# Performance work log

Hardware: AMD Instinct MI355X
Metric: run time of the kernel (lower is better)

Reference implementation:

```python
import jax, jax.numpy as jnp
import numpy as np
from jax import lax

B, NE, ZD, GAMMA, BETA = 16384, 512, 32, 0.99, 1.0

def conv2d(x, w, b, stride, pad):
    y = lax.conv_general_dilated(x, w, (stride, stride), [(pad, pad), (pad, pad)],
                                 dimension_numbers=('NCHW', 'OIHW', 'NCHW'))
    return y if b is None else y + b[None, :, None, None]

def convt2d(x, w, b, stride, pad):
    # torch ConvTranspose2d(w: [in,out,kh,kw]) == dilated conv with flipped, transposed kernel
    k = w.shape[2]
    wf = jnp.flip(w, (2, 3)).transpose(1, 0, 2, 3)  # -> [out,in,kh,kw]
    p = k - 1 - pad
    y = lax.conv_general_dilated(x, wf, (1, 1), [(p, p), (p, p)], lhs_dilation=(stride, stride),
                                 dimension_numbers=('NCHW', 'OIHW', 'NCHW'))
    return y + b[None, :, None, None]

def res_stack(x, w1, w2):
    # ResidualLayer: relu -> conv3x3 (32->64) -> relu -> conv1x1 (64->32), add; stack ends with relu
    r = jax.nn.relu(x)
    r = conv2d(r, w1, None, 1, 1)
    r = jax.nn.relu(r)
    r = conv2d(r, w2, None, 1, 0)
    return jax.nn.relu(x + r)

def linear(x, w, b):
    return x @ w.T + b

def setup_inputs() -> dict:
    key = jax.random.key(0)
    ks = jax.random.split(key, 24)
    g = lambda k, s, sc=0.05: (jax.random.normal(k, s) * sc).astype(jnp.float32)
    inp = {
        'x': jax.random.uniform(ks[0], (B, 1, 28, 28), dtype=jnp.float32),
        'conv1_w': g(ks[1], (16, 1, 4, 4)), 'conv1_b': jnp.zeros((16,), jnp.float32),
        'conv2_w': g(ks[2], (32, 16, 4, 4)), 'conv2_b': jnp.zeros((32,), jnp.float32),
        'res1_w1': g(ks[3], (64, 32, 3, 3)), 'res1_w2': g(ks[4], (32, 64, 1, 1)),
        'fc1_w': g(ks[5], (224, 1568)), 'fc1_b': jnp.zeros((224,), jnp.float32),
        'fc2_w': g(ks[6], (ZD, 224)), 'fc2_b': jnp.zeros((ZD,), jnp.float32),
        'emb': jax.random.uniform(ks[7], (NE, ZD), jnp.float32, -1.0 / NE, 1.0 / NE),
        'n_mat': jnp.ones((NE,), jnp.float32),
        'm_mat': jnp.ones((NE, ZD), jnp.float32),
        'fc3_w': g(ks[8], (224, ZD)), 'fc3_b': jnp.zeros((224,), jnp.float32),
        'fc4_w': g(ks[9], (1568, 224)), 'fc4_b': jnp.zeros((1568,), jnp.float32),
        'res2_w1': g(ks[10], (64, 32, 3, 3)), 'res2_w2': g(ks[11], (32, 64, 1, 1)),
        'convt1_w': g(ks[12], (32, 16, 4, 4)), 'convt1_b': jnp.zeros((16,), jnp.float32),
        'convt2_w': g(ks[13], (16, 1, 4, 4)), 'convt2_b': jnp.zeros((1,), jnp.float32),
    }
    return inp

def vq(z, emb, n_mat, m_mat):
    # z: [N, ZD]; nearest-codeword assignment
    d = (jnp.sum(z * z, 1, keepdims=True) + jnp.sum(emb * emb, 1)
         - 2.0 * (z @ emb.T))                                   # [N, NE]
    idx = jnp.argmin(d, axis=1)                                  # [N]
    z_q = jnp.take(emb, idx, axis=0)                             # [N, ZD]
    counts = jax.ops.segment_sum(jnp.ones((z.shape[0],), z.dtype), idx, num_segments=NE)
    sums = jax.ops.segment_sum(lax.stop_gradient(z), idx, num_segments=NE)
    n_new = n_mat * GAMMA + counts * (1.0 - GAMMA)
    m_new = m_mat * GAMMA + sums * (1.0 - GAMMA)
    emb_new = m_new / n_new[:, None]
    commit_loss = BETA * jnp.mean((lax.stop_gradient(z_q) - z) ** 2)
    quant_loss = jnp.mean((z_q - lax.stop_gradient(z)) ** 2)
    z_q_st = z + lax.stop_gradient(z_q - z)                      # straight-through
    e_mean = counts / z.shape[0]
    perplexity = jnp.exp(-jnp.sum(e_mean * jnp.log(e_mean + 1e-10)))
    return quant_loss, commit_loss, z_q_st, perplexity, emb_new

def reference(x, conv1_w, conv1_b, conv2_w, conv2_b, res1_w1, res1_w2,
              fc1_w, fc1_b, fc2_w, fc2_b, emb, n_mat, m_mat,
              fc3_w, fc3_b, fc4_w, fc4_b, res2_w1, res2_w2,
              convt1_w, convt1_b, convt2_w, convt2_b):
    # encoder: 28x28 -> 14x14 -> 7x7
    h = jax.nn.relu(conv2d(x, conv1_w, conv1_b, 2, 1))
    h = conv2d(h, conv2_w, conv2_b, 2, 1)
    h = res_stack(h, res1_w1, res1_w2)
    h = h.reshape(h.shape[0], -1)                                # [B, 1568]
    h = jax.nn.relu(linear(h, fc1_w, fc1_b))
    z = linear(h, fc2_w, fc2_b)                                  # [B, ZD]
    quant_loss, commit_loss, z_q, perplexity, emb_new = vq(z, emb, n_mat, m_mat)
    # decoder
    h = jax.nn.relu(linear(z_q, fc3_w, fc3_b))
    h = jax.nn.relu(linear(h, fc4_w, fc4_b))
    h = h.reshape(-1, 32, 7, 7)
    h = res_stack(h, res2_w1, res2_w2)
    h = jax.nn.relu(convt2d(h, convt1_w, convt1_b, 2, 1))
    x_rec = convt2d(h, convt2_w, convt2_b, 2, 1)                 # [B,1,28,28]
    return x_rec, quant_loss, commit_loss, perplexity, emb_new
```

## Files before the change

### kernel.cpp

```cpp
#include <hip/hip_runtime.h>
#include <math.h>

#define NB 16384
typedef unsigned short ushort_t;
typedef unsigned int uint_t;
typedef __attribute__((ext_vector_type(8))) short short8;
typedef __attribute__((ext_vector_type(4))) float fx4;
typedef _Float16 half2v __attribute__((ext_vector_type(2)));
typedef _Float16 half4v __attribute__((ext_vector_type(4)));

static const size_t OFF_HB    = 0;
static const size_t OFF_F1B   = 12845056;
static const size_t OFF_F3B   = 14680064;
static const size_t OFF_Z     = 16515072;
static const size_t OFF_IDX   = 17039360;
static const size_t OFF_ZQB   = 17055744;
static const size_t OFF_CNT   = 17317888;
static const size_t OFF_SUM   = 17318400;
static const size_t OFF_LOSS  = 17334784;
static const size_t OFF_WENC  = 17334848;
static const size_t OFF_WT1B  = 17343040;
static const size_t OFF_WR1B  = 17351232;
static const size_t OFF_WR2B  = 17360448;
static const size_t OFF_W2B1  = 17369664;
static const size_t OFF_W2B2  = 17370688;
static const size_t OFF_FC1WB = 17371712;
static const size_t OFF_FC2WB = 17547328;
static const size_t OFF_FC3WB = 17550912;
static const size_t OFF_FC4WB = 17554496;
static const size_t OFF_FC4BP = 17730112;

static __device__ __forceinline__ ushort_t f2bf(float f) {
  union { float f; uint_t u; } v; v.f = f;
  return (ushort_t)((v.u + 0x7fffu + ((v.u >> 16) & 1u)) >> 16);
}
static __device__ __forceinline__ float bf2f(ushort_t h) {
  union { uint_t u; float f; } v; v.u = ((uint_t)h) << 16;
  return v.f;
}
static __device__ __forceinline__ float fdot2(half2v a, half2v b, float c) {
#if __has_builtin(__builtin_amdgcn_fdot2)
  return __builtin_amdgcn_fdot2(a, b, c, false);
#else
  return c + (float)a.x * (float)b.x + (float)a.y * (float)b.y;
#endif
}

__global__ __launch_bounds__(256) void k_prep(
    const float* __restrict__ c2w, const float* __restrict__ r1w1,
    const float* __restrict__ r1w2, const float* __restrict__ r2w1,
    const float* __restrict__ r2w2, const float* __restrict__ t1w,
    const float* __restrict__ fc1w, const float* __restrict__ fc2w,
    const float* __restrict__ fc3w, const float* __restrict__ fc4w,
    const float* __restrict__ fc4b, float* __restrict__ ws)
{
  int gid = blockIdx.x * 256 + threadIdx.x;
  if (gid == 0) ws[OFF_LOSS] = 0.f;
  if (gid >= 775712) return;
  ushort_t* wencb = (ushort_t*)(ws + OFF_WENC);
  ushort_t* wt1b  = (ushort_t*)(ws + OFF_WT1B);
  ushort_t* wr1b  = (ushort_t*)(ws + OFF_WR1B);
  ushort_t* wr2b  = (ushort_t*)(ws + OFF_WR2B);
  ushort_t* w2b1  = (ushort_t*)(ws + OFF_W2B1);
  ushort_t* w2b2  = (ushort_t*)(ws + OFF_W2B2);
  ushort_t* fc1wb = (ushort_t*)(ws + OFF_FC1WB);
  ushort_t* fc2wb = (ushort_t*)(ws + OFF_FC2WB);
  ushort_t* fc3wb = (ushort_t*)(ws + OFF_FC3WB);
  ushort_t* fc4wb = (ushort_t*)(ws + OFF_FC4WB);
  float*    fc4bp = ws + OFF_FC4BP;
  int i = gid;
  if (i < 8192) {
    int kidx = i & 31, rest = i >> 5, co = rest & 31, kb = rest >> 5;
    int ky = kb >> 1, k2 = kb & 1, kxs = kidx >> 4, ci = kidx & 15;
    wencb[i] = f2bf(c2w[co*256 + ci*16 + ky*4 + 2*k2 + kxs]);
  } else if (i < 16384) {
    int j = i - 8192, ci = j & 31, rest = j >> 5, co = rest & 15, kk = rest >> 4;
    wt1b[j] = f2bf(t1w[ci*256 + co*16 + kk]);
  } else if (i < 34816) {
    int j = i - 16384, ci = j & 31, r = j >> 5, co = r & 63, kk = r >> 6;
    wr1b[j] = f2bf(r1w1[co*288 + ci*9 + kk]);
  } else if (i < 53248) {
    int j = i - 34816, ci = j & 31, r = j >> 5, co = r & 63, kk = r >> 6;
    wr2b[j] = f2bf(r2w1[co*288 + ci*9 + kk]);
  } else if (i < 55296) {
    int j = i - 53248; w2b1[j] = f2bf(r1w2[j]);
  } else if (i < 57344) {
    int j = i - 55296; w2b2[j] = f2bf(r2w2[j]);
  } else if (i < 408576) {
    int j = i - 57344, n = j / 1568, k = j % 1568;
    int p = k >> 5, ci = k & 31;
    fc1wb[j] = f2bf(fc1w[n*1568 + ci*49 + p]);
  } else if (i < 415744) {
    int j = i - 408576; fc2wb[j] = f2bf(fc2w[j]);
  } else if (i < 422912) {
    int j = i - 415744; fc3wb[j] = f2bf(fc3w[j]);
  } else if (i < 774144) {
    int j = i - 422912, np = j / 224, k = j % 224;
    int p = np >> 5, ci = np & 31;
    fc4wb[j] = f2bf(fc4w[(ci*49 + p)*224 + k]);
  } else {
    int np = i - 774144, p = np >> 5, ci = np & 31;
    fc4bp[np] = fc4b[ci*49 + p];
  }
}

__global__ __launch_bounds__(256) void k_enc(const float* __restrict__ x,
    const float* __restrict__ w1, const float* __restrict__ b1,
    const ushort_t* __restrict__ wencb, const float* __restrict__ b2,
    ushort_t* __restrict__ hb)
{
  __shared__ float xin[30][32];
  __shared__ ushort_t ph1b[256*24];
  __shared__ ushort_t outl[1568];
  int b = blockIdx.x, t = threadIdx.x, l = t & 63, w = t >> 6;
  int pr = l & 15, g = l >> 4;
  int co16 = t & 15;
  float wr1v[16];
  #pragma unroll
  for (int kk = 0; kk < 16; ++kk) wr1v[kk] = w1[co16*16 + kk];
  float bv1 = b1[co16];
  short8 bf[8][2];
  #pragma unroll
  for (int kb = 0; kb < 8; ++kb)
    #pragma unroll
    for (int nt = 0; nt < 2; ++nt)
      bf[kb][nt] = *(const short8*)(wencb + (size_t)(kb*32 + nt*16 + pr)*32 + g*8);
  uint_t* pz = (uint_t*)ph1b;
  for (int i = t; i < 3072; i += 256) pz[i] = 0;
  float* xp = &xin[0][0];
  for (int i = t; i < 960; i += 256) xp[i] = 0.f;
  __syncthreads();
  const float* xb = x + (size_t)b*784;
  for (int i = t; i < 784; i += 256) xin[i/28 + 1][i%28 + 1] = xb[i];
  __syncthreads();
  char* phc = (char*)ph1b;
  for (int i = t; i < 3136; i += 256) {
    int p = i >> 4, oy = p/14, ox = p%14;
    float acc = bv1;
    #pragma unroll
    for (int ky = 0; ky < 4; ++ky)
      #pragma unroll
      for (int kx = 0; kx < 4; ++kx)
        acc += xin[2*oy+ky][2*ox+kx] * wr1v[ky*4+kx];
    *(ushort_t*)(phc + ((oy+1)*16 + (ox+1))*48 + co16*2) = f2bf(fmaxf(acc, 0.f));
  }
  __syncthreads();
  int p = w*16 + pr; if (p > 48) p = 48;
  int oy = p/7, ox = p%7;
  fx4 acc2[2];
  acc2[0] = (fx4){0.f,0.f,0.f,0.f}; acc2[1] = (fx4){0.f,0.f,0.f,0.f};
  #pragma unroll
  for (int kb = 0; kb < 8; ++kb) {
    int ky = kb >> 1, k2 = kb & 1;
    int prow = (2*oy + ky)*16 + 2*ox + 2*k2 + (g >> 1);
    short8 afr = *(const short8*)(phc + prow*48 + (g & 1)*16);
    acc2[0] = __builtin_amdgcn_mfma_f32_16x16x32_bf16(afr, bf[kb][0], acc2[0], 0, 0, 0);
    acc2[1] = __builtin_amdgcn_mfma_f32_16x16x32_bf16(afr, bf[kb][1], acc2[1], 0, 0, 0);
  }
  #pragma unroll
  for (int nt = 0; nt < 2; ++nt) {
    int co = nt*16 + pr;
    float bv = b2[co];
    #pragma unroll
    for (int i = 0; i < 4; ++i) {
      int pix = w*16 + g*4 + i;
      if (pix < 49) outl[pix*32 + co] = f2bf(acc2[nt][i] + bv);
    }
  }
  __syncthreads();
  uint_t* dst = (uint_t*)(hb + (size_t)b*1568);
  const uint_t* so = (const uint_t*)outl;
  for (int j = t; j < 784; j += 256) dst[j] = so[j];
}

__global__ __launch_bounds__(256) void k_res(ushort_t* __restrict__ hb,
    const ushort_t* __restrict__ wrb, const ushort_t* __restrict__ w2b)
{
  __shared__ ushort_t pinT[3456];
  __shared__ ushort_t rl[4096];
  __shared__ ushort_t hrawb[1568];
  __shared__ ushort_t outl[1568];
  int b = blockIdx.x, t = threadIdx.x, l = t & 63, w = t >> 6, g = l >> 4;

  short8 bfr[9];
  #pragma unroll
  for (int o = 0; o < 9; ++o)
    bfr[o] = *(const short8*)(wrb + (size_t)(o*64 + w*16 + (l & 15))*32 + g*8);

  uint_t* pz = (uint_t*)pinT;
  for (int i = t; i < 1728; i += 256) pz[i] = 0;
  __syncthreads();

  const uint_t* src = (const uint_t*)(hb + (size_t)b*1568);
  char* pinc = (char*)pinT;
  for (int j = t; j < 784; j += 256) {
    uint_t u = src[j];
    ((uint_t*)hrawb)[j] = u;
    uint_t ur = u;
    ur = (ur & 0x80000000u) ? (ur & 0x0000ffffu) : ur;
    ur = (ur & 0x8000u)     ? (ur & 0xffff0000u) : ur;
    int p = j >> 4, c2 = (j & 15) << 1;
    int ppix = (p/7 + 1)*12 + (p%7) + 1;
    int byte = ((ppix << 6) + (c2 << 1)) ^ ((ppix & 6) << 3);
    *(uint_t*)(pinc + byte) = ur;
  }
  __syncthreads();

  fx4 acc[4];
  #pragma unroll
  for (int mt = 0; mt < 4; ++mt) acc[mt] = (fx4){0.f, 0.f, 0.f, 0.f};
  int pb[4];
  #pragma unroll
  for (int mt = 0; mt < 4; ++mt) {
    int p = mt*16 + (l & 15); if (p > 48) p = 48;
    pb[mt] = (p / 7)*12 + (p % 7);
  }
  #pragma unroll
  for (int mt = 0; mt < 4; ++mt) {
    #pragma unroll
    for (int o = 0; o < 9; ++o) {
      int ppix = pb[mt] + (o / 3)*12 + (o % 3);
      int byte = ((ppix << 6) + (g << 4)) ^ ((ppix & 6) << 3);
      short8 afr = *(const short8*)(pinc + byte);
      acc[mt] = __builtin_amdgcn_mfma_f32_16x16x32_bf16(afr, bfr[o], acc[mt], 0, 0, 0);
    }
  }
  char* rlc = (char*)rl;
  #pragma unroll
  for (int mt = 0; mt < 4; ++mt) {
    #pragma unroll
    for (int i = 0; i < 4; ++i) {
      int pixr = mt*16 + g*4 + i;
      int co2 = w*16 + (l & 15);
      int byte = ((pixr << 7) + (co2 << 1)) ^ ((pixr & 7) << 4);
      *(ushort_t*)(rlc + byte) = f2bf(fmaxf(acc[mt][i], 0.f));
    }
  }
  __syncthreads();

  fx4 a1[2];
  a1[0] = (fx4){0.f,0.f,0.f,0.f}; a1[1] = (fx4){0.f,0.f,0.f,0.f};
  int prr = w*16 + (l & 15);
  #pragma unroll
  for (int kf = 0; kf < 2; ++kf) {
    int byte = ((prr << 7) + (kf << 6) + (g << 4)) ^ ((prr & 7) << 4);
    short8 ar = *(const short8*)(rlc + byte);
    #pragma unroll
    for (int nt = 0; nt < 2; ++nt) {
      short8 br = *(const short8*)(w2b + (size_t)(nt*16 + (l & 15))*64 + kf*32 + g*8);
      a1[nt] = __builtin_amdgcn_mfma_f32_16x16x32_bf16(ar, br, a1[nt], 0, 0, 0);
    }
  }
  #pragma unroll
  for (int nt = 0; nt < 2; ++nt) {
    #pragma unroll
    for (int i = 0; i < 4; ++i) {
      int pix = w*16 + g*4 + i;
      if (pix < 49) {
        int co2 = nt*16 + (l & 15);
        int idx2 = pix*32 + co2;
        float v = bf2f(hrawb[idx2]) + a1[nt][i];
        outl[idx2] = f2bf(fmaxf(v, 0.f));
      }
    }
  }
  __syncthreads();
  uint_t* dst = (uint_t*)(hb + (size_t)b*1568);
  const uint_t* so = (const uint_t*)outl;
  for (int j = t; j < 784; j += 256) dst[j] = so[j];
}

template<int BNF, bool OUTBF16, bool RELU>
__global__ __launch_bounds__(256) void k_mm(const ushort_t* __restrict__ A,
    const ushort_t* __restrict__ Wb, const float* __restrict__ bias,
    void* __restrict__ C, int M, int N, int K)
{
  __shared__ ushort_t As[2048];
  int t = threadIdx.x, l = t & 63, w = t >> 6, g = l >> 4;
  int m0 = blockIdx.x * 64, n0 = blockIdx.y * (BNF * 16);
  fx4 acc[BNF];
  #pragma unroll
  for (int nt = 0; nt < BNF; ++nt) acc[nt] = (fx4){0.f, 0.f, 0.f, 0.f};
  char* asc = (char*)As;
  int srow = t >> 2, sks = (t & 3) * 8;
  int sbyte = ((srow << 6) + (sks << 1)) ^ ((srow & 6) << 3);
  int arow = w*16 + (l & 15);
  int abyte = ((arow << 6) + (g << 4)) ^ ((arow & 6) << 3);
  const ushort_t* ap = A + (size_t)(m0 + srow)*K + sks;
  short8 av = *(const short8*)ap;
  for (int k0 = 0; k0 < K; k0 += 32) {
    __syncthreads();
    *(short8*)(asc + sbyte) = av;
    __syncthreads();
    if (k0 + 32 < K) av = *(const short8*)(ap + k0 + 32);
    short8 afr = *(const short8*)(asc + abyte);
    #pragma unroll
    for (int nt = 0; nt < BNF; ++nt) {
      short8 bfr = *(const short8*)(Wb + (size_t)(n0 + nt*16 + (l & 15))*K + k0 + g*8);
      acc[nt] = __builtin_amdgcn_mfma_f32_16x16x32_bf16(afr, bfr, acc[nt], 0, 0, 0);
    }
  }
  #pragma unroll
  for (int nt = 0; nt < BNF; ++nt) {
    int col = n0 + nt*16 + (l & 15);
    float bv = bias[col];
    #pragma unroll
    for (int i = 0; i < 4; ++i) {
      int row = m0 + w*16 + g*4 + i;
      float v = acc[nt][i] + bv;
      if (RELU) v = fmaxf(v, 0.f);
      if (OUTBF16) ((ushort_t*)C)[(size_t)row*N + col] = f2bf(v);
      else         ((float*)C)[(size_t)row*N + col] = v;
    }
  }
}

__global__ __launch_bounds__(256) void k_vq_assign(const float* __restrict__ z,
    const float* __restrict__ emb, ushort_t* __restrict__ zqb, int* __restrict__ idx,
    float* __restrict__ loss)
{
  __shared__ float esq[512];
  int t = threadIdx.x;
  int n = blockIdx.x * 256 + t;
  for (int e = t; e < 512; e += 256) {
    const float4* ep = (const float4*)&emb[e*32];
    float s = 0.f;
    #pragma unroll
    for (int q = 0; q < 8; ++q) { float4 v = ep[q]; s += v.x*v.x + v.y*v.y + v.z*v.z + v.w*v.w; }
    esq[e] = s;
  }
  __syncthreads();
  float zv[32];
  const float4* zp = (const float4*)&z[n*32];
  float zz = 0.f;
  #pragma unroll
  for (int q = 0; q < 8; ++q) {
    float4 v = zp[q];
    zv[4*q]=v.x; zv[4*q+1]=v.y; zv[4*q+2]=v.z; zv[4*q+3]=v.w;
    zz += v.x*v.x + v.y*v.y + v.z*v.z + v.w*v.w;
  }
  float best = 3.4e38f; int bi = 0;
  for (int e = 0; e < 512; ++e) {
    const float4* ep = (const float4*)&emb[e*32];
    float dot = 0.f;
    #pragma unroll
    for (int q = 0; q < 8; ++q) {
      float4 v = ep[q];
      dot += zv[4*q]*v.x + zv[4*q+1]*v.y + zv[4*q+2]*v.z + zv[4*q+3]*v.w;
    }
    float d = zz + esq[e] - 2.f*dot;
    if (d < best) { best = d; bi = e; }
  }
  idx[n] = bi;
  const float4* bp = (const float4*)&emb[bi*32];
  uint_t* zo = (uint_t*)(zqb + (size_t)n*32);
  float ls = 0.f;
  #pragma unroll
  for (int q = 0; q < 8; ++q) {
    float4 v = bp[q];
    zo[q*2]   = (uint_t)f2bf(v.x) | ((uint_t)f2bf(v.y) << 16);
    zo[q*2+1] = (uint_t)f2bf(v.z) | ((uint_t)f2bf(v.w) << 16);
    float d0 = v.x - zv[4*q], d1 = v.y - zv[4*q+1];
    float d2 = v.z - zv[4*q+2], d3 = v.w - zv[4*q+3];
    ls += d0*d0 + d1*d1 + d2*d2 + d3*d3;
  }
  #pragma unroll
  for (int m = 32; m >= 1; m >>= 1) ls += __shfl_xor(ls, m);
  if ((t & 63) == 0) atomicAdd(loss, ls);
}

__global__ __launch_bounds__(64) void k_vq_reduce(const int* __restrict__ idx,
    const float* __restrict__ z, float* __restrict__ counts, float* __restrict__ sums)
{
  int e = blockIdx.x, t = threadIdx.x;
  float cnt = 0.f, sv[32];
  #pragma unroll
  for (int k = 0; k < 32; ++k) sv[k] = 0.f;
  for (int n = t; n < 16384; n += 64) {
    if (idx[n] == e) {
      cnt += 1.f;
      const float4* zp = (const float4*)&z[n*32];
      #pragma unroll
      for (int q = 0; q < 8; ++q) {
        float4 v = zp[q];
        sv[4*q] += v.x; sv[4*q+1] += v.y; sv[4*q+2] += v.z; sv[4*q+3] += v.w;
      }
    }
  }
  #pragma unroll
  for (int m = 32; m >= 1; m >>= 1) {
    cnt += __shfl_xor(cnt, m);
    #pragma unroll
    for (int k = 0; k < 32; ++k) sv[k] += __shfl_xor(sv[k], m);
  }
  if (t == 0) {
    counts[e] = cnt;
    #pragma unroll
    for (int k = 0; k < 32; ++k) sums[e*32 + k] = sv[k];
  }
}

__global__ __launch_bounds__(512) void k_vq_final(const float* __restrict__ counts,
    const float* __restrict__ sums, const float* __restrict__ n_mat,
    const float* __restrict__ m_mat, const float* __restrict__ loss,
    float* __restrict__ out)
{
  __shared__ float red[8];
  int t = threadIdx.x;
  float c = counts[t];
  float nn = n_mat[t]*0.99f + c*0.01f;
  #pragma unroll
  for (int k = 0; k < 32; ++k) {
    float mn = m_mat[t*32+k]*0.99f + sums[t*32+k]*0.01f;
    out[12845059 + t*32 + k] = mn / nn;
  }
  float em = c * (1.f/16384.f);
  float ht = em * logf(em + 1e-10f);
  #pragma unroll
  for (int m = 32; m >= 1; m >>= 1) ht += __shfl_xor(ht, m);
  if ((t & 63) == 0) red[t >> 6] = ht;
  __syncthreads();
  if (t == 0) {
    float H = 0.f;
    #pragma unroll
    for (int i = 0; i < 8; ++i) H += red[i];
    float q = loss[0] * (1.f/524288.f);
    out[12845056] = q;
    out[12845057] = q;
    out[12845058] = expf(-H);
  }
}

__global__ __launch_bounds__(256) void k_dec(const ushort_t* __restrict__ h5,
    const ushort_t* __restrict__ wt1b, const float* __restrict__ bt1,
    const float* __restrict__ wt2, const float* __restrict__ bt2,
    float* __restrict__ out)
{
  __shared__ ushort_t pinT[3456];
  __shared__ ushort_t pt1b[256*20];
  __shared__ float w2l[256];
  __shared__ float outl[784];
  int b = blockIdx.x, t = threadIdx.x, l = t & 63, w = t >> 6;
  int pr = l & 15, g = l >> 4;
  int py = w >> 1, px = w & 1;
  short8 bfr[4];
  #pragma unroll
  for (int r = 0; r < 2; ++r)
    #pragma unroll
    for (int c = 0; c < 2; ++c) {
      int kk = (3 - py - 2*r)*4 + (3 - px - 2*c);
      bfr[r*2 + c] = *(const short8*)(wt1b + (size_t)(kk*16 + pr)*32 + g*8);
    }
  uint_t* pz = (uint_t*)pinT;
  for (int i = t; i < 1728; i += 256) pz[i] = 0;
  uint_t* qz = (uint_t*)pt1b;
  for (int i = t; i < 2560; i += 256) qz[i] = 0;
  if (t < 256) w2l[t] = wt2[t];
  __syncthreads();
  const uint_t* src = (const uint_t*)(h5 + (size_t)b*1568);
  char* pinc = (char*)pinT;
  for (int j = t; j < 784; j += 256) {
    uint_t u = src[j];
    int p = j >> 4, c2 = (j & 15) << 1;
    int ppix = (p/7 + 1)*12 + (p%7) + 1;
    int byte = ((ppix << 6) + (c2 << 1)) ^ ((ppix & 6) << 3);
    *(uint_t*)(pinc + byte) = u;
  }
  __syncthreads();
  fx4 acc[4];
  #pragma unroll
  for (int mt = 0; mt < 4; ++mt) acc[mt] = (fx4){0.f, 0.f, 0.f, 0.f};
  int pb[4];
  #pragma unroll
  for (int mt = 0; mt < 4; ++mt) {
    int p = mt*16 + pr; if (p > 48) p = 48;
    pb[mt] = (p / 7)*12 + (p % 7);
  }
  #pragma unroll
  for (int mt = 0; mt < 4; ++mt) {
    #pragma unroll
    for (int r = 0; r < 2; ++r)
      #pragma unroll
      for (int c = 0; c < 2; ++c) {
        int ppix = pb[mt] + (py + r)*12 + (px + c);
        int byte = ((ppix << 6) + (g << 4)) ^ ((ppix & 6) << 3);
        short8 afr = *(const short8*)(pinc + byte);
        acc[mt] = __builtin_amdgcn_mfma_f32_16x16x32_bf16(afr, bfr[r*2 + c], acc[mt], 0, 0, 0);
      }
  }
  char* ptc = (char*)pt1b;
  float bv1 = bt1[pr];
  #pragma unroll
  for (int mt = 0; mt < 4; ++mt) {
    #pragma unroll
    for (int i = 0; i < 4; ++i) {
      int p = mt*16 + g*4 + i;
      if (p < 49) {
        int yy = p / 7, xx = p % 7;
        int opix = (2*yy + py + 1)*16 + (2*xx + px + 1);
        *(_Float16*)(ptc + opix*40 + pr*2) = (_Float16)(fmaxf(acc[mt][i] + bv1, 0.f));
      }
    }
  }
  __syncthreads();
  {
    int qy = w >> 1, qx = w & 1;
    int kkt[4] = { qy*4 + qx, qy*4 + qx + 2, (qy+2)*4 + qx, (qy+2)*4 + qx + 2 };
    half2v wh[4][8];
    #pragma unroll
    for (int tt = 0; tt < 4; ++tt)
      #pragma unroll
      for (int q = 0; q < 8; ++q) {
        wh[tt][q].x = (_Float16)w2l[(2*q)*16 + kkt[tt]];
        wh[tt][q].y = (_Float16)w2l[(2*q+1)*16 + kkt[tt]];
      }
    float bv2 = bt2[0];
    #pragma unroll
    for (int k = 0; k < 4; ++k) {
      int j = l + k*64;
      if (j < 196) {
        int a = j / 14, bb = j % 14;
        int oy = 2*a + 1 - qy, ox = 2*bb + 1 - qx;
        int iy1 = a + 1 - qy, iy2 = a - qy;
        int ix1 = bb + 1 - qx, ix2 = bb - qx;
        int prw[4];
        prw[0] = (iy1 + 1)*16 + (ix1 + 1);
        prw[1] = (iy1 + 1)*16 + (ix2 + 1);
        prw[2] = (iy2 + 1)*16 + (ix1 + 1);
        prw[3] = (iy2 + 1)*16 + (ix2 + 1);
        float s = bv2;
        #pragma unroll
        for (int tt = 0; tt < 4; ++tt) {
          const char* base = ptc + prw[tt]*40;
          #pragma unroll
          for (int jj = 0; jj < 2; ++jj) {
            half4v a4 = *(const half4v*)(base + jj*8);
            half4v b4 = *(const half4v*)(base + 16 + jj*8);
            half2v a0 = {a4.x, a4.y}, a1 = {a4.z, a4.w};
            half2v b0 = {b4.x, b4.y}, b1 = {b4.z, b4.w};
            s = fdot2(a0, wh[tt][jj*2],     s);
            s = fdot2(a1, wh[tt][jj*2 + 1], s);
            s = fdot2(b0, wh[tt][jj*2 + 4], s);
            s = fdot2(b1, wh[tt][jj*2 + 5], s);
          }
        }
        outl[oy*28 + ox] = s;
      }
    }
  }
  __syncthreads();
  float* dst = out + (size_t)b*784;
  for (int i = t; i < 784; i += 256) dst[i] = outl[i];
}

extern "C" void kernel_launch(void* const* d_in, const int* in_sizes, int n_in,
                              void* d_out, int out_size, void* d_ws, size_t ws_size,
                              hipStream_t stream)
{
  const float* x    = (const float*)d_in[0];
  const float* c1w  = (const float*)d_in[1];
  const float* c1b  = (const float*)d_in[2];
  const float* c2w  = (const float*)d_in[3];
  const float* c2b  = (const float*)d_in[4];
  const float* r1w1 = (const float*)d_in[5];
  const float* r1w2 = (const float*)d_in[6];
  const float* fc1w = (const float*)d_in[7];
  const float* fc1b = (const float*)d_in[8];
  const float* fc2w = (const float*)d_in[9];
  const float* fc2b = (const float*)d_in[10];
  const float* emb  = (const float*)d_in[11];
  const float* nmat = (const float*)d_in[12];
  const float* mmat = (const float*)d_in[13];
  const float* fc3w = (const float*)d_in[14];
  const float* fc3b = (const float*)d_in[15];
  const float* fc4w = (const float*)d_in[16];
  const float* fc4b = (const float*)d_in[17];
  const float* r2w1 = (const float*)d_in[18];
  const float* r2w2 = (const float*)d_in[19];
  const float* t1w  = (const float*)d_in[20];
  const float* t1b  = (const float*)d_in[21];
  const float* t2w  = (const float*)d_in[22];
  const float* t2b  = (const float*)d_in[23];
  float* ws  = (float*)d_ws;
  float* out = (float*)d_out;

  ushort_t* hb   = (ushort_t*)(ws + OFF_HB);
  ushort_t* f1b  = (ushort_t*)(ws + OFF_F1B);
  ushort_t* f3b  = (ushort_t*)(ws + OFF_F3B);
  float*    z    = ws + OFF_Z;
  int*      idx  = (int*)(ws + OFF_IDX);
  ushort_t* zqb  = (ushort_t*)(ws + OFF_ZQB);
  float*    cnts = ws + OFF_CNT;
  float*    sums = ws + OFF_SUM;
  float*    loss = ws + OFF_LOSS;
  ushort_t* wencb = (ushort_t*)(ws + OFF_WENC);
  ushort_t* wt1b  = (ushort_t*)(ws + OFF_WT1B);
  ushort_t* wr1b  = (ushort_t*)(ws + OFF_WR1B);
  ushort_t* wr2b  = (ushort_t*)(ws + OFF_WR2B);
  ushort_t* w2b1  = (ushort_t*)(ws + OFF_W2B1);
  ushort_t* w2b2  = (ushort_t*)(ws + OFF_W2B2);
  ushort_t* fc1wb = (ushort_t*)(ws + OFF_FC1WB);
  ushort_t* fc2wb = (ushort_t*)(ws + OFF_FC2WB);
  ushort_t* fc3wb = (ushort_t*)(ws + OFF_FC3WB);
  ushort_t* fc4wb = (ushort_t*)(ws + OFF_FC4WB);
  float*    fc4bp = ws + OFF_FC4BP;

  k_prep<<<3031, 256, 0, stream>>>(c2w, r1w1, r1w2, r2w1, r2w2, t1w,
                                   fc1w, fc2w, fc3w, fc4w, fc4b, ws);
  k_enc<<<NB, 256, 0, stream>>>(x, c1w, c1b, wencb, c2b, hb);
  k_res<<<NB, 256, 0, stream>>>(hb, wr1b, w2b1);
  k_mm<14, true, true><<<dim3(256, 1), 256, 0, stream>>>(hb, fc1wb, fc1b, f1b, 16384, 224, 1568);
  k_mm<2, false, false><<<dim3(256, 1), 256, 0, stream>>>(f1b, fc2wb, fc2b, z, 16384, 32, 224);
  k_vq_assign<<<64, 256, 0, stream>>>(z, emb, zqb, idx, loss);
  k_vq_reduce<<<512, 64, 0, stream>>>(idx, z, cnts, sums);
  k_vq_final<<<1, 512, 0, stream>>>(cnts, sums, nmat, mmat, loss, out);
  k_mm<14, true, true><<<dim3(256, 1), 256, 0, stream>>>(zqb, fc3wb, fc3b, f3b, 16384, 224, 32);
  k_mm<14, true, true><<<dim3(256, 7), 256, 0, stream>>>(f3b, fc4wb, fc4bp, hb, 16384, 1568, 224);
  k_res<<<NB, 256, 0, stream>>>(hb, wr2b, w2b2);
  k_dec<<<NB, 256, 0, stream>>>(hb, wt1b, t1b, t2w, t2b, out);
}
```

Before: 994.3 us.

## Use MFMA for encoder conv1 and parallelize VQ assignment across wavefront lanes

The first encoder convolution now builds a bf16 im2col tile in swizzled shared memory and runs it as a 16x16x32 MFMA against a prepacked, zero-padded conv1 weight matrix, replacing the scalar FMA loop. The VQ nearest-codebook search changes from one thread per sample over 64 blocks to one wavefront per sample over 4096 blocks. Each lane scores 8 codes and the wave does a shuffle argmin with lowest-index tie-break. The goal is to remove the heavily underoccupied serial VQ kernel and the scalar conv work, at the cost of recomputing codebook norms per wave and running conv1 in bf16.

```diff
diff --git a/kernel.cpp b/kernel.cpp
--- a/kernel.cpp
+++ b/kernel.cpp
@@ -29,6 +29,7 @@
 static const size_t OFF_FC3WB = 17550912;
 static const size_t OFF_FC4WB = 17554496;
 static const size_t OFF_FC4BP = 17730112;
+static const size_t OFF_WENC1 = 17731680;
 
 static __device__ __forceinline__ ushort_t f2bf(float f) {
   union { float f; uint_t u; } v; v.f = f;
@@ -47,16 +48,17 @@
 }
 
 __global__ __launch_bounds__(256) void k_prep(
-    const float* __restrict__ c2w, const float* __restrict__ r1w1,
-    const float* __restrict__ r1w2, const float* __restrict__ r2w1,
-    const float* __restrict__ r2w2, const float* __restrict__ t1w,
+    const float* __restrict__ c1w, const float* __restrict__ c2w,
+    const float* __restrict__ r1w1, const float* __restrict__ r1w2,
+    const float* __restrict__ r2w1, const float* __restrict__ r2w2,
+    const float* __restrict__ t1w,
     const float* __restrict__ fc1w, const float* __restrict__ fc2w,
     const float* __restrict__ fc3w, const float* __restrict__ fc4w,
     const float* __restrict__ fc4b, float* __restrict__ ws)
 {
   int gid = blockIdx.x * 256 + threadIdx.x;
   if (gid == 0) ws[OFF_LOSS] = 0.f;
-  if (gid >= 775712) return;
+  if (gid >= 776224) return;
   ushort_t* wencb = (ushort_t*)(ws + OFF_WENC);
   ushort_t* wt1b  = (ushort_t*)(ws + OFF_WT1B);
   ushort_t* wr1b  = (ushort_t*)(ws + OFF_WR1B);
@@ -68,6 +70,7 @@
   ushort_t* fc3wb = (ushort_t*)(ws + OFF_FC3WB);
   ushort_t* fc4wb = (ushort_t*)(ws + OFF_FC4WB);
   float*    fc4bp = ws + OFF_FC4BP;
+  ushort_t* wenc1b = (ushort_t*)(ws + OFF_WENC1);
   int i = gid;
   if (i < 8192) {
     int kidx = i & 31, rest = i >> 5, co = rest & 31, kb = rest >> 5;
@@ -98,33 +101,36 @@
     int j = i - 422912, np = j / 224, k = j % 224;
     int p = np >> 5, ci = np & 31;
     fc4wb[j] = f2bf(fc4w[(ci*49 + p)*224 + k]);
-  } else {
+  } else if (i < 775712) {
     int np = i - 774144, p = np >> 5, ci = np & 31;
     fc4bp[np] = fc4b[ci*49 + p];
+  } else {
+    int j = i - 775712, k = j & 31, co = j >> 5;
+    wenc1b[j] = (k < 16) ? f2bf(c1w[co*16 + k]) : (ushort_t)0;
   }
 }
 
 __global__ __launch_bounds__(256) void k_enc(const float* __restrict__ x,
-    const float* __restrict__ w1, const float* __restrict__ b1,
+    const ushort_t* __restrict__ wenc1b, const float* __restrict__ b1,
     const ushort_t* __restrict__ wencb, const float* __restrict__ b2,
     ushort_t* __restrict__ hb)
 {
   __shared__ float xin[30][32];
+  __shared__ ushort_t icb[208*32];
   __shared__ ushort_t ph1b[256*24];
   __shared__ ushort_t outl[1568];
   int b = blockIdx.x, t = threadIdx.x, l = t & 63, w = t >> 6;
   int pr = l & 15, g = l >> 4;
-  int co16 = t & 15;
-  float wr1v[16];
-  #pragma unroll
-  for (int kk = 0; kk < 16; ++kk) wr1v[kk] = w1[co16*16 + kk];
-  float bv1 = b1[co16];
+  short8 bf1 = *(const short8*)(wenc1b + (size_t)pr*32 + g*8);
   short8 bf[8][2];
   #pragma unroll
   for (int kb = 0; kb < 8; ++kb)
     #pragma unroll
     for (int nt = 0; nt < 2; ++nt)
       bf[kb][nt] = *(const short8*)(wencb + (size_t)(kb*32 + nt*16 + pr)*32 + g*8);
+  float bv1 = b1[pr];
+  uint_t* iz = (uint_t*)icb;
+  for (int i = t; i < 3328; i += 256) iz[i] = 0;
   uint_t* pz = (uint_t*)ph1b;
   for (int i = t; i < 3072; i += 256) pz[i] = 0;
   float* xp = &xin[0][0];
@@ -133,16 +139,33 @@
   const float* xb = x + (size_t)b*784;
   for (int i = t; i < 784; i += 256) xin[i/28 + 1][i%28 + 1] = xb[i];
   __syncthreads();
+  char* icc = (char*)icb;
+  for (int i = t; i < 3136; i += 256) {
+    int p = i >> 4, k = i & 15;
+    int oy = p / 14, ox = p % 14;
+    float v = xin[2*oy + (k >> 2)][2*ox + (k & 3)];
+    int byte = ((p << 6) + (k << 1)) ^ ((p & 6) << 3);
+    *(ushort_t*)(icc + byte) = f2bf(v);
+  }
+  __syncthreads();
   char* phc = (char*)ph1b;
-  for (int i = t; i < 3136; i += 256) {
-    int p = i >> 4, oy = p/14, ox = p%14;
-    float acc = bv1;
-    #pragma unroll
-    for (int ky = 0; ky < 4; ++ky)
-      #pragma unroll
-      for (int kx = 0; kx < 4; ++kx)
-        acc += xin[2*oy+ky][2*ox+kx] * wr1v[ky*4+kx];
-    *(ushort_t*)(phc + ((oy+1)*16 + (ox+1))*48 + co16*2) = f2bf(fmaxf(acc, 0.f));
+  #pragma unroll
+  for (int mq = 0; mq < 4; ++mq) {
+    int mt = w + mq*4;
+    if (mt > 12) continue;
+    fx4 a1 = (fx4){0.f, 0.f, 0.f, 0.f};
+    int arow = mt*16 + pr;
+    int byte = ((arow << 6) + (g << 4)) ^ ((arow & 6) << 3);
+    short8 af = *(const short8*)(icc + byte);
+    a1 = __builtin_amdgcn_mfma_f32_16x16x32_bf16(af, bf1, a1, 0, 0, 0);
+    #pragma unroll
+    for (int i = 0; i < 4; ++i) {
+      int pix = mt*16 + g*4 + i;
+      if (pix < 196) {
+        int prow = (pix/14 + 1)*16 + (pix%14) + 1;
+        *(ushort_t*)(phc + prow*48 + pr*2) = f2bf(fmaxf(a1[i] + bv1, 0.f));
+      }
+    }
   }
   __syncthreads();
   int p = w*16 + pr; if (p > 48) p = 48;
@@ -319,19 +342,11 @@
     const float* __restrict__ emb, ushort_t* __restrict__ zqb, int* __restrict__ idx,
     float* __restrict__ loss)
 {
-  __shared__ float esq[512];
-  int t = threadIdx.x;
-  int n = blockIdx.x * 256 + t;
-  for (int e = t; e < 512; e += 256) {
-    const float4* ep = (const float4*)&emb[e*32];
-    float s = 0.f;
-    #pragma unroll
-    for (int q = 0; q < 8; ++q) { float4 v = ep[q]; s += v.x*v.x + v.y*v.y + v.z*v.z + v.w*v.w; }
-    esq[e] = s;
-  }
-  __syncthreads();
+  __shared__ float lred[4];
+  int t = threadIdx.x, w = t >> 6, ln = t & 63;
+  int n = blockIdx.x * 4 + w;
   float zv[32];
-  const float4* zp = (const float4*)&z[n*32];
+  const float4* zp = (const float4*)&z[(size_t)n*32];
   float zz = 0.f;
   #pragma unroll
   for (int q = 0; q < 8; ++q) {
@@ -339,34 +354,40 @@
     zv[4*q]=v.x; zv[4*q+1]=v.y; zv[4*q+2]=v.z; zv[4*q+3]=v.w;
     zz += v.x*v.x + v.y*v.y + v.z*v.z + v.w*v.w;
   }
-  float best = 3.4e38f; int bi = 0;
-  for (int e = 0; e < 512; ++e) {
-    const float4* ep = (const float4*)&emb[e*32];
-    float dot = 0.f;
+  float best = 3.4e38f; int bi = 0x7fffffff;
+  #pragma unroll
+  for (int c = 0; c < 8; ++c) {
+    int e = c*64 + ln;
+    const float4* ep = (const float4*)&emb[(size_t)e*32];
+    float dot = 0.f, es = 0.f;
     #pragma unroll
     for (int q = 0; q < 8; ++q) {
       float4 v = ep[q];
       dot += zv[4*q]*v.x + zv[4*q+1]*v.y + zv[4*q+2]*v.z + zv[4*q+3]*v.w;
-    }
-    float d = zz + esq[e] - 2.f*dot;
+      es  += v.x*v.x + v.y*v.y + v.z*v.z + v.w*v.w;
+    }
+    float d = zz + es - 2.f*dot;
     if (d < best) { best = d; bi = e; }
   }
-  idx[n] = bi;
-  const float4* bp = (const float4*)&emb[bi*32];
-  uint_t* zo = (uint_t*)(zqb + (size_t)n*32);
+  #pragma unroll
+  for (int m = 32; m >= 1; m >>= 1) {
+    float ob = __shfl_xor(best, m);
+    int   oi = __shfl_xor(bi, m);
+    if (ob < best || (ob == best && oi < bi)) { best = ob; bi = oi; }
+  }
+  if (ln == 0) idx[n] = bi;
+  int dim = ln & 31;
+  float ev = emb[(size_t)bi*32 + dim];
+  float evh = __shfl_xor(ev, 1);
+  if (ln < 32 && !(ln & 1))
+    ((uint_t*)(zqb + (size_t)n*32))[ln >> 1] = (uint_t)f2bf(ev) | ((uint_t)f2bf(evh) << 16);
   float ls = 0.f;
-  #pragma unroll
-  for (int q = 0; q < 8; ++q) {
-    float4 v = bp[q];
-    zo[q*2]   = (uint_t)f2bf(v.x) | ((uint_t)f2bf(v.y) << 16);
-    zo[q*2+1] = (uint_t)f2bf(v.z) | ((uint_t)f2bf(v.w) << 16);
-    float d0 = v.x - zv[4*q], d1 = v.y - zv[4*q+1];
-    float d2 = v.z - zv[4*q+2], d3 = v.w - zv[4*q+3];
-    ls += d0*d0 + d1*d1 + d2*d2 + d3*d3;
-  }
+  if (ln < 32) { float d = ev - z[(size_t)n*32 + dim]; ls = d*d; }
   #pragma unroll
   for (int m = 32; m >= 1; m >>= 1) ls += __shfl_xor(ls, m);
-  if ((t & 63) == 0) atomicAdd(loss, ls);
+  if (ln == 0) lred[w] = ls;
+  __syncthreads();
+  if (t == 0) atomicAdd(loss, lred[0] + lred[1] + lred[2] + lred[3]);
 }
 
 __global__ __launch_bounds__(64) void k_vq_reduce(const int* __restrict__ idx,
@@ -593,25 +614,26 @@
   float*    cnts = ws + OFF_CNT;
   float*    sums = ws + OFF_SUM;
   float*    loss = ws + OFF_LOSS;
-  ushort_t* wencb = (ushort_t*)(ws + OFF_WENC);
-  ushort_t* wt1b  = (ushort_t*)(ws + OFF_WT1B);
-  ushort_t* wr1b  = (ushort_t*)(ws + OFF_WR1B);
-  ushort_t* wr2b  = (ushort_t*)(ws + OFF_WR2B);
-  ushort_t* w2b1  = (ushort_t*)(ws + OFF_W2B1);
-  ushort_t* w2b2  = (ushort_t*)(ws + OFF_W2B2);
-  ushort_t* fc1wb = (ushort_t*)(ws + OFF_FC1WB);
-  ushort_t* fc2wb = (ushort_t*)(ws + OFF_FC2WB);
-  ushort_t* fc3wb = (ushort_t*)(ws + OFF_FC3WB);
-  ushort_t* fc4wb = (ushort_t*)(ws + OFF_FC4WB);
-  float*    fc4bp = ws + OFF_FC4BP;
-
-  k_prep<<<3031, 256, 0, stream>>>(c2w, r1w1, r1w2, r2w1, r2w2, t1w,
+  ushort_t* wencb  = (ushort_t*)(ws + OFF_WENC);
+  ushort_t* wenc1b = (ushort_t*)(ws + OFF_WENC1);
+  ushort_t* wt1b   = (ushort_t*)(ws + OFF_WT1B);
+  ushort_t* wr1b   = (ushort_t*)(ws + OFF_WR1B);
+  ushort_t* wr2b   = (ushort_t*)(ws + OFF_WR2B);
+  ushort_t* w2b1   = (ushort_t*)(ws + OFF_W2B1);
+  ushort_t* w2b2   = (ushort_t*)(ws + OFF_W2B2);
+  ushort_t* fc1wb  = (ushort_t*)(ws + OFF_FC1WB);
+  ushort_t* fc2wb  = (ushort_t*)(ws + OFF_FC2WB);
+  ushort_t* fc3wb  = (ushort_t*)(ws + OFF_FC3WB);
+  ushort_t* fc4wb  = (ushort_t*)(ws + OFF_FC4WB);
+  float*    fc4bp  = ws + OFF_FC4BP;
+
+  k_prep<<<3033, 256, 0, stream>>>(c1w, c2w, r1w1, r1w2, r2w1, r2w2, t1w,
                                    fc1w, fc2w, fc3w, fc4w, fc4b, ws);
-  k_enc<<<NB, 256, 0, stream>>>(x, c1w, c1b, wencb, c2b, hb);
+  k_enc<<<NB, 256, 0, stream>>>(x, wenc1b, c1b, wencb, c2b, hb);
   k_res<<<NB, 256, 0, stream>>>(hb, wr1b, w2b1);
   k_mm<14, true, true><<<dim3(256, 1), 256, 0, stream>>>(hb, fc1wb, fc1b, f1b, 16384, 224, 1568);
   k_mm<2, false, false><<<dim3(256, 1), 256, 0, stream>>>(f1b, fc2wb, fc2b, z, 16384, 32, 224);
-  k_vq_assign<<<64, 256, 0, stream>>>(z, emb, zqb, idx, loss);
+  k_vq_assign<<<4096, 256, 0, stream>>>(z, emb, zqb, idx, loss);
   k_vq_reduce<<<512, 64, 0, stream>>>(idx, z, cnts, sums);
   k_vq_final<<<1, 512, 0, stream>>>(cnts, sums, nmat, mmat, loss, out);
   k_mm<14, true, true><<<dim3(256, 1), 256, 0, stream>>>(zqb, fc3wb, fc3b, f3b, 16384, 224, 32);
```

Measured after the change: 1.029 ms. 1.03x slower.

## Split VQ codebook search across warps with LDS-staged embeddings

Applied to the files above, without the earlier changes.

The nearest-codebook search now launches 256 blocks of 512 threads instead of 64 blocks of 256. The full embedding table and a 64-row tile of z are staged in shared memory. Each of 8 wavefronts scans 64 codes for the same 64 rows, and the partial argmins are merged in LDS with ties broken toward the lower index. This targets the previous low occupancy, where each thread serially scanned 512 codes from global memory. In exchange it uses about 70KB of LDS per block and adds several barriers.

```diff
diff --git a/kernel.cpp b/kernel.cpp
--- a/kernel.cpp
+++ b/kernel.cpp
@@ -315,58 +315,87 @@
   }
 }
 
-__global__ __launch_bounds__(256) void k_vq_assign(const float* __restrict__ z,
+__global__ __launch_bounds__(512) void k_vq_assign(const float* __restrict__ z,
     const float* __restrict__ emb, ushort_t* __restrict__ zqb, int* __restrict__ idx,
     float* __restrict__ loss)
 {
+  __shared__ float embL[16384];
   __shared__ float esq[512];
-  int t = threadIdx.x;
-  int n = blockIdx.x * 256 + t;
-  for (int e = t; e < 512; e += 256) {
-    const float4* ep = (const float4*)&emb[e*32];
+  __shared__ float zL[64*33];
+  __shared__ float bestdL[8][64];
+  __shared__ int   bestiL[8][64];
+  int t = threadIdx.x, r = t & 63, q = t >> 6;
+  int n0 = blockIdx.x * 64;
+  fx4* embL4 = (fx4*)embL;
+  const fx4* emb4 = (const fx4*)emb;
+  #pragma unroll
+  for (int j = 0; j < 8; ++j) embL4[t + j*512] = emb4[t + j*512];
+  {
+    int f0 = t*4;
+    int row = f0 >> 5, col = f0 & 31;
+    const float4 v = *(const float4*)&z[(size_t)n0*32 + f0];
+    zL[row*33 + col]   = v.x; zL[row*33 + col+1] = v.y;
+    zL[row*33 + col+2] = v.z; zL[row*33 + col+3] = v.w;
+  }
+  __syncthreads();
+  {
     float s = 0.f;
-    #pragma unroll
-    for (int q = 0; q < 8; ++q) { float4 v = ep[q]; s += v.x*v.x + v.y*v.y + v.z*v.z + v.w*v.w; }
-    esq[e] = s;
-  }
-  __syncthreads();
+    const fx4* ep = (const fx4*)&embL[t*32 & 16383];
+    #pragma unroll
+    for (int j2 = 0; j2 < 8; ++j2) { fx4 v = ep[j2]; s += v.x*v.x + v.y*v.y + v.z*v.z + v.w*v.w; }
+    esq[t & 511] = s;
+  }
   float zv[32];
-  const float4* zp = (const float4*)&z[n*32];
-  float zz = 0.f;
-  #pragma unroll
-  for (int q = 0; q < 8; ++q) {
-    float4 v = zp[q];
-    zv[4*q]=v.x; zv[4*q+1]=v.y; zv[4*q+2]=v.z; zv[4*q+3]=v.w;
-    zz += v.x*v.x + v.y*v.y + v.z*v.z + v.w*v.w;
-  }
+  #pragma unroll
+  for (int k = 0; k < 32; ++k) zv[k] = zL[r*33 + k];
+  __syncthreads();
   float best = 3.4e38f; int bi = 0;
-  for (int e = 0; e < 512; ++e) {
-    const float4* ep = (const float4*)&emb[e*32];
+  for (int j = 0; j < 64; ++j) {
+    int e = q*64 + j;
+    const fx4* ep = (const fx4*)&embL[e*32];
     float dot = 0.f;
     #pragma unroll
-    for (int q = 0; q < 8; ++q) {
-      float4 v = ep[q];
-      dot += zv[4*q]*v.x + zv[4*q+1]*v.y + zv[4*q+2]*v.z + zv[4*q+3]*v.w;
-    }
-    float d = zz + esq[e] - 2.f*dot;
+    for (int k2 = 0; k2 < 8; ++k2) {
+      fx4 v = ep[k2];
+      dot += zv[4*k2]*v.x + zv[4*k2+1]*v.y + zv[4*k2+2]*v.z + zv[4*k2+3]*v.w;
+    }
+    float d = esq[e] - 2.f*dot;
     if (d < best) { best = d; bi = e; }
   }
-  idx[n] = bi;
-  const float4* bp = (const float4*)&emb[bi*32];
-  uint_t* zo = (uint_t*)(zqb + (size_t)n*32);
-  float ls = 0.f;
-  #pragma unroll
-  for (int q = 0; q < 8; ++q) {
-    float4 v = bp[q];
-    zo[q*2]   = (uint_t)f2bf(v.x) | ((uint_t)f2bf(v.y) << 16);
-    zo[q*2+1] = (uint_t)f2bf(v.z) | ((uint_t)f2bf(v.w) << 16);
-    float d0 = v.x - zv[4*q], d1 = v.y - zv[4*q+1];
-    float d2 = v.z - zv[4*q+2], d3 = v.w - zv[4*q+3];
-    ls += d0*d0 + d1*d1 + d2*d2 + d3*d3;
-  }
-  #pragma unroll
-  for (int m = 32; m >= 1; m >>= 1) ls += __shfl_xor(ls, m);
-  if ((t & 63) == 0) atomicAdd(loss, ls);
+  bestdL[q][r] = best; bestiL[q][r] = bi;
+  __syncthreads();
+  if (t < 64) {
+    float bb = bestdL[0][r]; int bbi = bestiL[0][r];
+    #pragma unroll
+    for (int j = 1; j < 8; ++j) {
+      float d = bestdL[j][r]; int di = bestiL[j][r];
+      if (d < bb || (d == bb && di < bbi)) { bb = d; bbi = di; }
+    }
+    idx[n0 + r] = bbi;
+    bestiL[0][r] = bbi;
+  }
+  __syncthreads();
+  if (t < 256) {
+    int q4 = t >> 6;
+    int n = n0 + r;
+    int bsel = bestiL[0][r];
+    float ls = 0.f;
+    uint_t ow[4];
+    #pragma unroll
+    for (int h = 0; h < 4; ++h) {
+      float e0 = embL[bsel*32 + q4*8 + 2*h];
+      float e1 = embL[bsel*32 + q4*8 + 2*h + 1];
+      float d0 = e0 - zv[q4*8 + 2*h], d1 = e1 - zv[q4*8 + 2*h + 1];
+      ls += d0*d0 + d1*d1;
+      ow[h] = (uint_t)f2bf(e0) | ((uint_t)f2bf(e1) << 16);
+    }
+    uint_t* zo = (uint_t*)(zqb + (size_t)n*32) + q4*4;
+    #pragma unroll
+    for (int h = 0; h < 4; ++h) zo[h] = ow[h];
+    #pragma unroll
+    for (int m = 32; m >= 1; m >>= 1) ls += __shfl_xor(ls, m);
+    if (r == 0) atomicAdd(loss, ls);
+  }
 }
 
 __global__ __launch_bounds__(64) void k_vq_reduce(const int* __restrict__ idx,
@@ -593,17 +622,17 @@
   float*    cnts = ws + OFF_CNT;
   float*    sums = ws + OFF_SUM;
   float*    loss = ws + OFF_LOSS;
-  ushort_t* wencb = (ushort_t*)(ws + OFF_WENC);
-  ushort_t* wt1b  = (ushort_t*)(ws + OFF_WT1B);
-  ushort_t* wr1b  = (ushort_t*)(ws + OFF_WR1B);
-  ushort_t* wr2b  = (ushort_t*)(ws + OFF_WR2B);
-  ushort_t* w2b1  = (ushort_t*)(ws + OFF_W2B1);
-  ushort_t* w2b2  = (ushort_t*)(ws + OFF_W2B2);
-  ushort_t* fc1wb = (ushort_t*)(ws + OFF_FC1WB);
-  ushort_t* fc2wb = (ushort_t*)(ws + OFF_FC2WB);
-  ushort_t* fc3wb = (ushort_t*)(ws + OFF_FC3WB);
-  ushort_t* fc4wb = (ushort_t*)(ws + OFF_FC4WB);
-  float*    fc4bp = ws + OFF_FC4BP;
+  ushort_t* wencb  = (ushort_t*)(ws + OFF_WENC);
+  ushort_t* wt1b   = (ushort_t*)(ws + OFF_WT1B);
+  ushort_t* wr1b   = (ushort_t*)(ws + OFF_WR1B);
+  ushort_t* wr2b   = (ushort_t*)(ws + OFF_WR2B);
+  ushort_t* w2b1   = (ushort_t*)(ws + OFF_W2B1);
+  ushort_t* w2b2   = (ushort_t*)(ws + OFF_W2B2);
+  ushort_t* fc1wb  = (ushort_t*)(ws + OFF_FC1WB);
+  ushort_t* fc2wb  = (ushort_t*)(ws + OFF_FC2WB);
+  ushort_t* fc3wb  = (ushort_t*)(ws + OFF_FC3WB);
+  ushort_t* fc4wb  = (ushort_t*)(ws + OFF_FC4WB);
+  float*    fc4bp  = ws + OFF_FC4BP;
 
   k_prep<<<3031, 256, 0, stream>>>(c2w, r1w1, r1w2, r2w1, r2w2, t1w,
                                    fc1w, fc2w, fc3w, fc4w, fc4b, ws);
@@ -611,7 +640,7 @@
   k_res<<<NB, 256, 0, stream>>>(hb, wr1b, w2b1);
   k_mm<14, true, true><<<dim3(256, 1), 256, 0, stream>>>(hb, fc1wb, fc1b, f1b, 16384, 224, 1568);
   k_mm<2, false, false><<<dim3(256, 1), 256, 0, stream>>>(f1b, fc2wb, fc2b, z, 16384, 32, 224);
-  k_vq_assign<<<64, 256, 0, stream>>>(z, emb, zqb, idx, loss);
+  k_vq_assign<<<256, 512, 0, stream>>>(z, emb, zqb, idx, loss);
   k_vq_reduce<<<512, 64, 0, stream>>>(idx, z, cnts, sums);
   k_vq_final<<<1, 512, 0, stream>>>(cnts, sums, nmat, mmat, loss, out);
   k_mm<14, true, true><<<dim3(256, 1), 256, 0, stream>>>(zqb, fc3wb, fc3b, f3b, 16384, 224, 32);
```

Result: faster. 895.5 us (-9.9%).
